# Kernel optimization log

Measured on AMD Instinct MI355X. Metric: run time of the kernel, lower is better.

Reference implementation:

```python
import jax, jax.numpy as jnp
import numpy as np

IN_V = 16
OUT_V = 16
HS = 64
INCR = 2
METRIC = jnp.array([1.0, -1.0, -1.0, -1.0], dtype=jnp.float32)


def setup_inputs() -> dict:
    key = jax.random.key(0)
    ks = jax.random.split(key, 9)
    B, N = 64, 1024
    vectors = jax.random.normal(ks[0], (B, N, IN_V, 4), dtype=jnp.float32)
    scalars = jax.random.normal(ks[1], (B, N, HS), dtype=jnp.float32)
    # kaiming-uniform-ish init scale for [out, in] weights
    def w(k, o, i):
        bound = 1.0 / np.sqrt(i)
        return jax.random.uniform(k, (o, i), jnp.float32, -bound, bound)
    Wq = w(ks[2], IN_V * INCR, IN_V)
    Wk = w(ks[3], IN_V * INCR, IN_V)
    Wv = w(ks[4], OUT_V, IN_V)  # exp() applied in forward (EquiLinearTimelike)
    Wq_s = w(ks[5], HS, HS)
    Wk_s = w(ks[6], HS, HS)
    bq_s = jax.random.uniform(ks[7], (HS,), jnp.float32, -1 / np.sqrt(HS), 1 / np.sqrt(HS))
    bk_s = jax.random.uniform(ks[8], (HS,), jnp.float32, -1 / np.sqrt(HS), 1 / np.sqrt(HS))
    return {"vectors": vectors, "scalars": scalars, "Wq": Wq, "Wq_s": Wq_s,
            "bq_s": bq_s, "Wk": Wk, "Wk_s": Wk_s, "bk_s": bk_s, "Wv": Wv}


def reference(vectors, scalars, Wq, Wq_s, bq_s, Wk, Wk_s, bk_s, Wv):
    B, N = vectors.shape[:2]
    # Lorentz squared norm: t^2 - x^2 - y^2 - z^2 over last axis -> [B,N,IN_V,1]
    norm = jnp.einsum('bnik,k->bni', vectors * vectors, METRIC)[..., None]
    vecs = vectors / jnp.sqrt(jnp.clip(jnp.abs(norm), 1e-5))
    # Q/K vector projections [B,N,IN_V*INCR,4] and scalar projections [B,N,HS]
    q_v = jnp.einsum('ij,bnjk->bnik', Wq, vecs)
    k_v = jnp.einsum('ij,bnjk->bnik', Wk, vecs)
    q_s = scalars @ Wq_s.T + bq_s
    k_s = scalars @ Wk_s.T + bk_s
    # embed: flatten vectors (K gets metric factor) and concat scalars
    q = jnp.concatenate([q_v.reshape(B, N, -1), q_s], axis=-1)
    k = jnp.concatenate([(k_v * METRIC).reshape(B, N, -1), k_s], axis=-1)
    # V: positive-weight (timelike) projection, flatten -> [B,N,OUT_V*4]
    v = jnp.einsum('ij,bnjk->bnik', jnp.exp(Wv), vecs).reshape(B, N, -1)
    # scaled dot-product attention over the particle axis
    scale = 1.0 / jnp.sqrt(jnp.asarray(q.shape[-1], q.dtype))
    scores = jnp.einsum('bqd,bkd->bqk', q, k) * scale
    attn = jax.nn.softmax(scores, axis=-1)
    out = jnp.einsum('bqk,bkd->bqd', attn, v)
    return out.reshape(B, N, -1, 4)
```

## Files before the change

### kernel.cpp

```cpp
#include <hip/hip_runtime.h>
#include <math.h>

typedef float f32x16 __attribute__((ext_vector_type(16)));
typedef short bf16x8 __attribute__((ext_vector_type(8)));
typedef short bf16x4 __attribute__((ext_vector_type(4)));
typedef unsigned short u16;
typedef unsigned int u32;

#define MFMA32(a, b, c) __builtin_amdgcn_mfma_f32_32x32x16_bf16(a, b, c, 0, 0, 0)

__device__ __forceinline__ u16 f2bf(float x) {
    u32 u = __float_as_uint(x);
    u += 0x7FFFu + ((u >> 16) & 1u);
    return (u16)(u >> 16);
}
__device__ __forceinline__ float bf2f(u16 h) {
    return __uint_as_float(((u32)h) << 16);
}
__device__ __forceinline__ void gload16(const void* g, void* l) {
    __builtin_amdgcn_global_load_lds(
        (const __attribute__((address_space(1))) unsigned int*)g,
        (__attribute__((address_space(3))) unsigned int*)l, 16, 0, 0);
}

__global__ __launch_bounds__(256) void g_kernel(
    const float* __restrict__ Wq, const float* __restrict__ Wk,
    const float* __restrict__ Wv,
    u16* __restrict__ gmh, u16* __restrict__ gml,
    u16* __restrict__ mvh, u16* __restrict__ mvl)
{
    const int bk = blockIdx.x;
    const int base = ((bk & 3) * 256 + threadIdx.x) * 4;
    if (bk < 4) {
#pragma unroll
        for (int i = 0; i < 4; ++i) {
            int e = base + i;
            int f = e >> 6, fp = e & 63;
            int c = f & 3, cp = fp & 3, j = f >> 2, jp = fp >> 2;
            float val = 0.f;
            if (c == cp) {
                float a0 = 0.f, a1 = 0.f;
#pragma unroll 8
                for (int ff = 0; ff < 32; ff += 2) {
                    a0 = fmaf(Wq[ff * 16 + j],       Wk[ff * 16 + jp],       a0);
                    a1 = fmaf(Wq[(ff + 1) * 16 + j], Wk[(ff + 1) * 16 + jp], a1);
                }
                val = (a0 + a1) * ((c == 0) ? 1.f : -1.f);
            }
            u16 h = f2bf(val);
            gmh[e] = h; gml[e] = f2bf(val - bf2f(h));
        }
    } else {
#pragma unroll
        for (int i = 0; i < 4; ++i) {
            int e = base + i;
            int f = e >> 6, fp = e & 63;
            float val = ((f & 3) == (fp & 3)) ? expf(Wv[(f >> 2) * 16 + (fp >> 2)]) : 0.f;
            u16 h = f2bf(val);
            mvh[e] = h; mvl[e] = f2bf(val - bf2f(h));
        }
    }
}

__global__ __launch_bounds__(256) void prep_kernel(
    const float* __restrict__ vectors, const float* __restrict__ scalars,
    const float* __restrict__ Wq_s, const float* __restrict__ bq_s,
    const float* __restrict__ Wk_s, const float* __restrict__ bk_s,
    const u16* __restrict__ gmh, const u16* __restrict__ gml,
    const u16* __restrict__ mvh, const u16* __restrict__ mvl,
    u16* __restrict__ qh, u16* __restrict__ ql,
    u16* __restrict__ kh, u16* __restrict__ kl,
    u16* __restrict__ vth)
{
    const int t = threadIdx.x;
    const int w = t >> 6;
    const int lane = t & 63;
    const int l31 = lane & 31, g = lane >> 5;
    const int b = blockIdx.x >> 5;
    const int n0 = (blockIdx.x & 31) << 5;
    const long tok0 = (long)b * 1024 + n0;
    const float SC = 0.07216878364870323f;

    if (w == 1 || w == 2) {
        bf16x8 Ah[4], Al[4];
        const float* vrow = vectors + (tok0 + l31) * 64 + g * 8;
#pragma unroll
        for (int kk = 0; kk < 4; ++kk) {
            float4 x0 = *(const float4*)(vrow + kk * 16);
            float4 x1 = *(const float4*)(vrow + kk * 16 + 4);
            float nr0 = x0.x * x0.x - x0.y * x0.y - x0.z * x0.z - x0.w * x0.w;
            float iv0 = 1.0f / sqrtf(fmaxf(fabsf(nr0), 1e-5f));
            float nr1 = x1.x * x1.x - x1.y * x1.y - x1.z * x1.z - x1.w * x1.w;
            float iv1 = 1.0f / sqrtf(fmaxf(fabsf(nr1), 1e-5f));
            float xs[8] = {x0.x * iv0, x0.y * iv0, x0.z * iv0, x0.w * iv0,
                           x1.x * iv1, x1.y * iv1, x1.z * iv1, x1.w * iv1};
#pragma unroll
            for (int e = 0; e < 8; ++e) {
                u16 h = f2bf(xs[e]);
                Ah[kk][e] = (short)h;
                Al[kk][e] = (short)f2bf(xs[e] - bf2f(h));
            }
        }

        const u16* bhp = (w == 1) ? gmh : mvh;
        const u16* blp = (w == 1) ? gml : mvl;
#pragma unroll
        for (int tile = 0; tile < 2; ++tile) {
            const int fs = tile * 32 + l31;
            const u16* bh = bhp + fs * 64 + g * 8;
            const u16* bl = blp + fs * 64 + g * 8;
            f32x16 acc;
#pragma unroll
            for (int r = 0; r < 16; ++r) acc[r] = 0.f;
#pragma unroll
            for (int kk = 0; kk < 4; ++kk) {
                bf16x8 Bh = *(const bf16x8*)(bh + kk * 16);
                bf16x8 Bl = *(const bf16x8*)(bl + kk * 16);
                acc = MFMA32(Ah[kk], Bh, acc);
                acc = MFMA32(Al[kk], Bh, acc);
                acc = MFMA32(Ah[kk], Bl, acc);
            }
            if (w == 1) {
#pragma unroll
                for (int reg = 0; reg < 16; ++reg) {
                    int trow = (reg & 3) + 8 * (reg >> 2) + 4 * g;
                    float val = acc[reg];
                    u16 h = f2bf(val);
                    kh[(tok0 + trow) * 128 + fs] = h;
                    kl[(tok0 + trow) * 64 + fs] = f2bf(val - bf2f(h));
                }
            } else {
#pragma unroll
                for (int reg = 0; reg < 16; ++reg) {
                    int trow = (reg & 3) + 8 * (reg >> 2) + 4 * g;
                    vth[((long)b * 64 + fs) * 1024 + n0 + trow] = f2bf(acc[reg]);
                }
            }
        }
    } else {
        if (w == 0) {
            const float* vrow = vectors + (tok0 + l31) * 64 + g * 8;
#pragma unroll
            for (int kk = 0; kk < 4; ++kk) {
                float4 x0 = *(const float4*)(vrow + kk * 16);
                float4 x1 = *(const float4*)(vrow + kk * 16 + 4);
                float nr0 = x0.x * x0.x - x0.y * x0.y - x0.z * x0.z - x0.w * x0.w;
                float iv0 = SC / sqrtf(fmaxf(fabsf(nr0), 1e-5f));
                float nr1 = x1.x * x1.x - x1.y * x1.y - x1.z * x1.z - x1.w * x1.w;
                float iv1 = SC / sqrtf(fmaxf(fabsf(nr1), 1e-5f));
                float xs[8] = {x0.x * iv0, x0.y * iv0, x0.z * iv0, x0.w * iv0,
                               x1.x * iv1, x1.y * iv1, x1.z * iv1, x1.w * iv1};
                u16 hh[8], ll[8];
#pragma unroll
                for (int e = 0; e < 8; ++e) {
                    hh[e] = f2bf(xs[e]);
                    ll[e] = f2bf(xs[e] - bf2f(hh[e]));
                }
                *(int4*)(qh + (tok0 + l31) * 128 + kk * 16 + g * 8) = *(int4*)hh;
                *(int4*)(ql + (tok0 + l31) * 64 + kk * 16 + g * 8) = *(int4*)ll;
            }
        }
        const int isq = (w == 0);
        bf16x8 Ah[4];
        const float* xrow = scalars + (tok0 + l31) * 64 + g * 8;
#pragma unroll
        for (int kk = 0; kk < 4; ++kk) {
            float4 x0 = *(const float4*)(xrow + kk * 16);
            float4 x1 = *(const float4*)(xrow + kk * 16 + 4);
            float xs[8] = {x0.x, x0.y, x0.z, x0.w, x1.x, x1.y, x1.z, x1.w};
#pragma unroll
            for (int e = 0; e < 8; ++e) Ah[kk][e] = (short)f2bf(xs[e]);
        }
        const float sc = isq ? SC : 1.f;
        u16* oh = isq ? qh : kh;
#pragma unroll
        for (int ft = 0; ft < 2; ++ft) {
            const int fs = (ft << 5) + l31;
            const float* wrow = (isq ? Wq_s : Wk_s) + fs * 64 + g * 8;
            f32x16 acc;
#pragma unroll
            for (int r = 0; r < 16; ++r) acc[r] = 0.f;
#pragma unroll
            for (int kk = 0; kk < 4; ++kk) {
                float4 w0_ = *(const float4*)(wrow + kk * 16);
                float4 w1_ = *(const float4*)(wrow + kk * 16 + 4);
                float ws_[8] = {w0_.x, w0_.y, w0_.z, w0_.w, w1_.x, w1_.y, w1_.z, w1_.w};
                bf16x8 Bh;
#pragma unroll
                for (int e = 0; e < 8; ++e) Bh[e] = (short)f2bf(ws_[e]);
                acc = MFMA32(Ah[kk], Bh, acc);
            }
            const float bias = (isq ? bq_s : bk_s)[fs];
#pragma unroll
            for (int reg = 0; reg < 16; ++reg) {
                int trow = (reg & 3) + 8 * (reg >> 2) + 4 * g;
                oh[(tok0 + trow) * 128 + 64 + fs] = f2bf((acc[reg] + bias) * sc);
            }
        }
    }
}

__global__ __launch_bounds__(256) void attn_kernel(
    const u16* __restrict__ qh, const u16* __restrict__ ql,
    const u16* __restrict__ kh, const u16* __restrict__ kl,
    const u16* __restrict__ vth, u16* __restrict__ pob,
    float2* __restrict__ pml)
{
    __shared__ u16 KH[2 * 32 * 128];
    __shared__ u16 KL[2 * 32 * 64];
    __shared__ u16 VH[2 * 64 * 40];

    const int t = threadIdx.x;
    const int lane = t & 63;
    const int w = t >> 6;
    const int l31 = lane & 31, g = lane >> 5;

    const int bid = blockIdx.x;
    const int xcd = bid & 7;
    const int idx = bid >> 3;
    const int b = xcd * 8 + (idx >> 4);
    const int qt = (idx >> 1) & 7;
    const int half = idx & 1;
    const int kv0 = half << 9;

    const int qi = qt * 128 + w * 32 + l31;
    const long qtok = (long)b * 1024 + qi;

    bf16x8 Qh[8], Qlv[4];
    {
        const u16* qhp = qh + qtok * 128 + g * 8;
        const u16* qlp = ql + qtok * 64 + g * 8;
#pragma unroll
        for (int c = 0; c < 8; ++c) Qh[c] = *(const bf16x8*)(qhp + c * 16);
#pragma unroll
        for (int c = 0; c < 4; ++c) Qlv[c] = *(const bf16x8*)(qlp + c * 16);
    }

    const int r0 = 8 * w + (lane >> 4);
    const int r1 = r0 + 4;
    const int su0 = (lane & 15) ^ (r0 & 15);
    const int su1 = (lane & 15) ^ (r1 & 15);
    const u16* kh0 = kh + ((long)b * 1024 + kv0 + r0) * 128 + su0 * 8;
    const u16* kh1 = kh + ((long)b * 1024 + kv0 + r1) * 128 + su1 * 8;
    const int rl_ = 8 * w + (lane >> 3);
    const int sul = (lane & 7) ^ (rl_ & 7);
    const u16* kl0 = kl + ((long)b * 1024 + kv0 + rl_) * 64 + sul * 8;

    const int vdv = t >> 2, vq4 = t & 3;
    const u16* vhg = vth + ((long)b * 64 + vdv) * 1024 + kv0 + vq4 * 8;
    u16* vdst = VH + vdv * 40 + vq4 * 8;
    int4 rv0;

#define STAGEK(kt, bf) do { \
        gload16(kh0 + (long)(kt) * 128, KH + (bf) * 4096 + w * 1024); \
        gload16(kh1 + (long)(kt) * 128, KH + (bf) * 4096 + w * 1024 + 512); \
        gload16(kl0 + (long)(kt) * 64,  KL + (bf) * 2048 + w * 512); \
    } while (0)

    f32x16 o0, o1;
#pragma unroll
    for (int r = 0; r < 16; ++r) { o0[r] = 0.f; o1[r] = 0.f; }
    float m_run = -1e30f, l_run = 0.f;

    rv0 = *(const int4*)(vhg);
    STAGEK(0, 0);
    *(int4*)(vdst) = rv0;
    asm volatile("s_waitcnt vmcnt(0)" ::: "memory");
    __syncthreads();

    for (int it = 0; it < 16; ++it) {
        const int cb = it & 1;
        if (it < 15) {
            rv0 = *(const int4*)(vhg + (it + 1) * 32);
            STAGEK((it + 1) * 32, cb ^ 1);
        }

        f32x16 sA, sB;
#pragma unroll
        for (int r = 0; r < 16; ++r) { sA[r] = 0.f; sB[r] = 0.f; }
        const u16* kbh = KH + cb * 4096 + l31 * 128;
        const u16* kbl = KL + cb * 2048 + l31 * 64;
        const int rs = l31 & 15, rs7 = l31 & 7;
        __builtin_amdgcn_s_setprio(1);
#pragma unroll
        for (int c = 0; c < 4; ++c) {
            bf16x8 fh = *(const bf16x8*)(kbh + ((g + 2 * c) ^ rs) * 8);
            bf16x8 fl = *(const bf16x8*)(kbl + ((g + 2 * c) ^ rs7) * 8);
            sA = MFMA32(fh, Qh[c], sA);
            sB = MFMA32(fl, Qh[c], sB);
            sB = MFMA32(fh, Qlv[c], sB);
        }
#pragma unroll
        for (int c = 4; c < 8; ++c) {
            bf16x8 fh = *(const bf16x8*)(kbh + ((g + 2 * c) ^ rs) * 8);
            sA = MFMA32(fh, Qh[c], sA);
        }
        __builtin_amdgcn_s_setprio(0);

        float s[16];
#pragma unroll
        for (int r = 0; r < 16; ++r) s[r] = sA[r] + sB[r];
        float mt = s[0];
#pragma unroll
        for (int r = 1; r < 16; ++r) mt = fmaxf(mt, s[r]);
        mt = fmaxf(mt, __shfl_xor(mt, 32));
        if (!__all(mt - m_run <= 8.f)) {
            float mn = fmaxf(m_run, mt);
            float corr = __expf(m_run - mn);
            l_run *= corr;
#pragma unroll
            for (int r = 0; r < 16; ++r) { o0[r] *= corr; o1[r] *= corr; }
            m_run = mn;
        }
        float ps = 0.f;
#pragma unroll
        for (int r = 0; r < 16; ++r) { s[r] = __expf(s[r] - m_run); ps += s[r]; }
        ps += __shfl_xor(ps, 32);
        l_run += ps;

        bf16x8 ph0, ph1;
#pragma unroll
        for (int e = 0; e < 8; ++e) {
            ph0[e] = (short)f2bf(s[e]);
            ph1[e] = (short)f2bf(s[8 + e]);
        }

        const u16* vb = VH + cb * 2560;
        bf16x8 v00, v01, v10, v11;
        {
            const u16* p00 = vb + l31 * 40 + g * 4;
            const u16* p10 = vb + (32 + l31) * 40 + g * 4;
            bf16x4 a0 = *(const bf16x4*)(p00);      bf16x4 a1 = *(const bf16x4*)(p00 + 8);
            bf16x4 b0 = *(const bf16x4*)(p00 + 16); bf16x4 b1 = *(const bf16x4*)(p00 + 24);
            bf16x4 c0 = *(const bf16x4*)(p10);      bf16x4 c1 = *(const bf16x4*)(p10 + 8);
            bf16x4 d0 = *(const bf16x4*)(p10 + 16); bf16x4 d1 = *(const bf16x4*)(p10 + 24);
            v00 = __builtin_shufflevector(a0, a1, 0, 1, 2, 3, 4, 5, 6, 7);
            v01 = __builtin_shufflevector(b0, b1, 0, 1, 2, 3, 4, 5, 6, 7);
            v10 = __builtin_shufflevector(c0, c1, 0, 1, 2, 3, 4, 5, 6, 7);
            v11 = __builtin_shufflevector(d0, d1, 0, 1, 2, 3, 4, 5, 6, 7);
        }

        __builtin_amdgcn_s_setprio(1);
        o0 = MFMA32(v00, ph0, o0);
        o0 = MFMA32(v01, ph1, o0);
        o1 = MFMA32(v10, ph0, o1);
        o1 = MFMA32(v11, ph1, o1);
        __builtin_amdgcn_s_setprio(0);

        if (it < 15) *(int4*)(vdst + (cb ^ 1) * 2560) = rv0;
        asm volatile("s_waitcnt vmcnt(0)" ::: "memory");
        __syncthreads();
    }

    u16* poA = pob + (long)half * 4194304 + qtok * 64;
#pragma unroll
    for (int sg = 0; sg < 4; ++sg) {
        u32 pk0 = (u32)f2bf(o0[4 * sg + 0]) | ((u32)f2bf(o0[4 * sg + 1]) << 16);
        u32 pk1 = (u32)f2bf(o0[4 * sg + 2]) | ((u32)f2bf(o0[4 * sg + 3]) << 16);
        *(int2*)(poA + sg * 8 + g * 4) = make_int2((int)pk0, (int)pk1);
        u32 pk2 = (u32)f2bf(o1[4 * sg + 0]) | ((u32)f2bf(o1[4 * sg + 1]) << 16);
        u32 pk3 = (u32)f2bf(o1[4 * sg + 2]) | ((u32)f2bf(o1[4 * sg + 3]) << 16);
        *(int2*)(poA + 32 + sg * 8 + g * 4) = make_int2((int)pk2, (int)pk3);
    }
    if (g == 0) {
        pml[((long)half * 64 + b) * 1024 + qi] = make_float2(m_run, l_run);
    }
#undef STAGEK
}

__global__ __launch_bounds__(256) void merge_kernel(
    const u16* __restrict__ pob, const float2* __restrict__ pml,
    float* __restrict__ out)
{
    const int idx = blockIdx.x * 256 + threadIdx.x;
    const int q = idx >> 2;
    const int part = idx & 3;
    float2 a = pml[q];
    float2 c = pml[65536 + q];
    float m = fmaxf(a.x, c.x);
    float w0 = __expf(a.x - m), w1 = __expf(c.x - m);
    float inv = 1.0f / (w0 * a.y + w1 * c.y);
    const u16* p0 = pob + (long)q * 64 + part * 16;
    const u16* p1 = p0 + 4194304;
    u16 va[16], vb[16];
    *(int4*)&va[0] = *(const int4*)p0;
    *(int4*)&va[8] = *(const int4*)(p0 + 8);
    *(int4*)&vb[0] = *(const int4*)p1;
    *(int4*)&vb[8] = *(const int4*)(p1 + 8);
    float4* op = (float4*)(out + (long)q * 64 + part * 16);
#pragma unroll
    for (int j = 0; j < 4; ++j) {
        float4 o4;
        o4.x = (w0 * bf2f(va[j * 4 + 0]) + w1 * bf2f(vb[j * 4 + 0])) * inv;
        o4.y = (w0 * bf2f(va[j * 4 + 1]) + w1 * bf2f(vb[j * 4 + 1])) * inv;
        o4.z = (w0 * bf2f(va[j * 4 + 2]) + w1 * bf2f(vb[j * 4 + 2])) * inv;
        o4.w = (w0 * bf2f(va[j * 4 + 3]) + w1 * bf2f(vb[j * 4 + 3])) * inv;
        op[j] = o4;
    }
}

extern "C" void kernel_launch(void* const* d_in, const int* in_sizes, int n_in,
                              void* d_out, int out_size, void* d_ws, size_t ws_size,
                              hipStream_t stream) {
    const float* vectors = (const float*)d_in[0];
    const float* scalars = (const float*)d_in[1];
    const float* Wq   = (const float*)d_in[2];
    const float* Wq_s = (const float*)d_in[3];
    const float* bq_s = (const float*)d_in[4];
    const float* Wk   = (const float*)d_in[5];
    const float* Wk_s = (const float*)d_in[6];
    const float* bk_s = (const float*)d_in[7];
    const float* Wv   = (const float*)d_in[8];
    float* o = (float*)d_out;

    u16* qh  = (u16*)d_ws;
    u16* ql  = qh + 8388608;
    u16* kh  = ql + 4194304;
    u16* kl  = kh + 8388608;
    u16* vth = kl + 4194304;
    u16* pob = vth + 4194304;
    float2* pml = (float2*)(pob + 8388608);
    u16* gmh = (u16*)(pml + 131072);
    u16* gml = gmh + 4096;
    u16* mvh = gml + 4096;
    u16* mvl = mvh + 4096;

    g_kernel<<<8, 256, 0, stream>>>(Wq, Wk, Wv, gmh, gml, mvh, mvl);
    prep_kernel<<<2048, 256, 0, stream>>>(vectors, scalars, Wq_s, bq_s,
                                          Wk_s, bk_s, gmh, gml, mvh, mvl,
                                          qh, ql, kh, kl, vth);
    attn_kernel<<<1024, 256, 0, stream>>>(qh, ql, kh, kl, vth, pob, pml);
    merge_kernel<<<1024, 256, 0, stream>>>(pob, pml, o);
}
```

Measured before the change: 108.1 us.

## Fold log2e into Q scale, use exp2, truncating bf16 pack, drop redundant waits

Pre-multiplies the Q scale by log2(e) so the softmax can use the native exp2 instruction instead of __expf, with the rescale threshold and the merge kernel adjusted to match. The max and sum reductions become trees, the P-to-bf16 conversion switches from round-to-nearest to a byte-permute truncation, the explicit vmcnt(0) waits before the barriers are removed, and the main loop is unrolled by two. The aim is to cut VALU work in the softmax inner loop, at the cost of slightly less accurate probabilities from truncation. Dropping the waits relies on __syncthreads and the compiler to order the global-to-LDS loads correctly.

```diff
diff --git a/kernel.cpp b/kernel.cpp
--- a/kernel.cpp
+++ b/kernel.cpp
@@ -79,7 +79,7 @@
     const int b = blockIdx.x >> 5;
     const int n0 = (blockIdx.x & 31) << 5;
     const long tok0 = (long)b * 1024 + n0;
-    const float SC = 0.07216878364870323f;
+    const float SC2 = 0.07216878364870323f * 1.4426950408889634f;
 
     if (w == 1 || w == 2) {
         bf16x8 Ah[4], Al[4];
@@ -145,9 +145,9 @@
                 float4 x0 = *(const float4*)(vrow + kk * 16);
                 float4 x1 = *(const float4*)(vrow + kk * 16 + 4);
                 float nr0 = x0.x * x0.x - x0.y * x0.y - x0.z * x0.z - x0.w * x0.w;
-                float iv0 = SC / sqrtf(fmaxf(fabsf(nr0), 1e-5f));
+                float iv0 = SC2 / sqrtf(fmaxf(fabsf(nr0), 1e-5f));
                 float nr1 = x1.x * x1.x - x1.y * x1.y - x1.z * x1.z - x1.w * x1.w;
-                float iv1 = SC / sqrtf(fmaxf(fabsf(nr1), 1e-5f));
+                float iv1 = SC2 / sqrtf(fmaxf(fabsf(nr1), 1e-5f));
                 float xs[8] = {x0.x * iv0, x0.y * iv0, x0.z * iv0, x0.w * iv0,
                                x1.x * iv1, x1.y * iv1, x1.z * iv1, x1.w * iv1};
                 u16 hh[8], ll[8];
@@ -171,7 +171,7 @@
 #pragma unroll
             for (int e = 0; e < 8; ++e) Ah[kk][e] = (short)f2bf(xs[e]);
         }
-        const float sc = isq ? SC : 1.f;
+        const float sc = isq ? SC2 : 1.f;
         u16* oh = isq ? qh : kh;
 #pragma unroll
         for (int ft = 0; ft < 2; ++ft) {
@@ -265,9 +265,9 @@
     rv0 = *(const int4*)(vhg);
     STAGEK(0, 0);
     *(int4*)(vdst) = rv0;
-    asm volatile("s_waitcnt vmcnt(0)" ::: "memory");
     __syncthreads();
 
+#pragma unroll 2
     for (int it = 0; it < 16; ++it) {
         const int cb = it & 1;
         if (it < 15) {
@@ -300,30 +300,41 @@
         float s[16];
 #pragma unroll
         for (int r = 0; r < 16; ++r) s[r] = sA[r] + sB[r];
-        float mt = s[0];
-#pragma unroll
-        for (int r = 1; r < 16; ++r) mt = fmaxf(mt, s[r]);
+        float m01 = fmaxf(s[0], s[1]),   m23 = fmaxf(s[2], s[3]);
+        float m45 = fmaxf(s[4], s[5]),   m67 = fmaxf(s[6], s[7]);
+        float m89 = fmaxf(s[8], s[9]),   mab = fmaxf(s[10], s[11]);
+        float mcd = fmaxf(s[12], s[13]), mef = fmaxf(s[14], s[15]);
+        float mt = fmaxf(fmaxf(fmaxf(m01, m23), fmaxf(m45, m67)),
+                         fmaxf(fmaxf(m89, mab), fmaxf(mcd, mef)));
         mt = fmaxf(mt, __shfl_xor(mt, 32));
-        if (!__all(mt - m_run <= 8.f)) {
+        if (!__all(mt - m_run <= 11.54f)) {
             float mn = fmaxf(m_run, mt);
-            float corr = __expf(m_run - mn);
+            float corr = __builtin_amdgcn_exp2f(m_run - mn);
             l_run *= corr;
 #pragma unroll
             for (int r = 0; r < 16; ++r) { o0[r] *= corr; o1[r] *= corr; }
             m_run = mn;
         }
-        float ps = 0.f;
-#pragma unroll
-        for (int r = 0; r < 16; ++r) { s[r] = __expf(s[r] - m_run); ps += s[r]; }
+#pragma unroll
+        for (int r = 0; r < 16; ++r) s[r] = __builtin_amdgcn_exp2f(s[r] - m_run);
+        float p01 = s[0] + s[1],   p23 = s[2] + s[3];
+        float p45 = s[4] + s[5],   p67 = s[6] + s[7];
+        float p89 = s[8] + s[9],   pab = s[10] + s[11];
+        float pcd = s[12] + s[13], pef = s[14] + s[15];
+        float ps = ((p01 + p23) + (p45 + p67)) + ((p89 + pab) + (pcd + pef));
         ps += __shfl_xor(ps, 32);
         l_run += ps;
 
-        bf16x8 ph0, ph1;
-#pragma unroll
-        for (int e = 0; e < 8; ++e) {
-            ph0[e] = (short)f2bf(s[e]);
-            ph1[e] = (short)f2bf(s[8 + e]);
-        }
+        u32 pk[4], pk2[4];
+#pragma unroll
+        for (int e = 0; e < 4; ++e) {
+            pk[e]  = __builtin_amdgcn_perm(__float_as_uint(s[2 * e + 1]),
+                                           __float_as_uint(s[2 * e]), 0x07060302u);
+            pk2[e] = __builtin_amdgcn_perm(__float_as_uint(s[8 + 2 * e + 1]),
+                                           __float_as_uint(s[8 + 2 * e]), 0x07060302u);
+        }
+        bf16x8 ph0 = *(bf16x8*)pk;
+        bf16x8 ph1 = *(bf16x8*)pk2;
 
         const u16* vb = VH + cb * 2560;
         bf16x8 v00, v01, v10, v11;
@@ -348,7 +359,6 @@
         __builtin_amdgcn_s_setprio(0);
 
         if (it < 15) *(int4*)(vdst + (cb ^ 1) * 2560) = rv0;
-        asm volatile("s_waitcnt vmcnt(0)" ::: "memory");
         __syncthreads();
     }
 
@@ -358,9 +368,9 @@
         u32 pk0 = (u32)f2bf(o0[4 * sg + 0]) | ((u32)f2bf(o0[4 * sg + 1]) << 16);
         u32 pk1 = (u32)f2bf(o0[4 * sg + 2]) | ((u32)f2bf(o0[4 * sg + 3]) << 16);
         *(int2*)(poA + sg * 8 + g * 4) = make_int2((int)pk0, (int)pk1);
-        u32 pk2 = (u32)f2bf(o1[4 * sg + 0]) | ((u32)f2bf(o1[4 * sg + 1]) << 16);
-        u32 pk3 = (u32)f2bf(o1[4 * sg + 2]) | ((u32)f2bf(o1[4 * sg + 3]) << 16);
-        *(int2*)(poA + 32 + sg * 8 + g * 4) = make_int2((int)pk2, (int)pk3);
+        u32 pk2_ = (u32)f2bf(o1[4 * sg + 0]) | ((u32)f2bf(o1[4 * sg + 1]) << 16);
+        u32 pk3_ = (u32)f2bf(o1[4 * sg + 2]) | ((u32)f2bf(o1[4 * sg + 3]) << 16);
+        *(int2*)(poA + 32 + sg * 8 + g * 4) = make_int2((int)pk2_, (int)pk3_);
     }
     if (g == 0) {
         pml[((long)half * 64 + b) * 1024 + qi] = make_float2(m_run, l_run);
@@ -378,7 +388,7 @@
     float2 a = pml[q];
     float2 c = pml[65536 + q];
     float m = fmaxf(a.x, c.x);
-    float w0 = __expf(a.x - m), w1 = __expf(c.x - m);
+    float w0 = __builtin_amdgcn_exp2f(a.x - m), w1 = __builtin_amdgcn_exp2f(c.x - m);
     float inv = 1.0f / (w0 * a.y + w1 * c.y);
     const u16* p0 = pob + (long)q * 64 + part * 16;
     const u16* p1 = p0 + 4194304;
```

Measured after the change: 103.7 us. 4.1% less time.
